# Performance work log

Hardware: AMD Instinct MI355X
Metric: run time of the kernel (lower is better)

## Reference

```python
import jax, jax.numpy as jnp
import numpy as np

# SLAYER SRM-ALPHA neuron / simulation constants (from netParams)
THETA = 10.0      # spike threshold
TAU_SR = 10.0     # PSP (SRM) time constant
TAU_REF = 1.0     # refractory time constant
SCALE_REF = 2.0
TAU_RHO = 1.0     # surrogate-gradient width (unused in fwd)
SCALE_RHO = 1.0
TS = 1.0
K_SRM = 100       # truncation of alpha kernel (values < 1e-4 beyond this)
K_REF = 16

def _alpha_kernel(tau, K, mult):
    t = jnp.arange(K, dtype=jnp.float32) * TS
    return mult * (t / tau) * jnp.exp(1.0 - t / tau)

SRM_KERNEL = _alpha_kernel(TAU_SR, K_SRM, 1.0)                       # eps(t)
REF_KERNEL = _alpha_kernel(TAU_REF, K_REF, -2.0 * THETA * SCALE_REF)  # nu(t)

def heaviside(u):
    return (u >= THETA).astype(u.dtype)

def psp(x):
    # causal temporal convolution with SRM alpha kernel; x: (..., T)
    T = x.shape[-1]
    K = SRM_KERNEL.shape[0]
    flat = x.reshape(-1, 1, T)  # (N, C=1, T)
    out = jax.lax.conv_general_dilated(flat, SRM_KERNEL[::-1].reshape(1, 1, K),
                                       (1,), [(K - 1, 0)])
    return out.reshape(x.shape)

def spike(v):
    # SLAYER spike generation with refractory feedback; v: (..., T)
    refk = REF_KERNEL[1:]          # refractory affects strictly future steps
    L = refk.shape[0]
    vT = jnp.moveaxis(v, -1, 0)    # (T, ...)
    pend0 = jnp.zeros(vT.shape[1:] + (L,), v.dtype)  # pending refractory contributions
    def step(pend, vt):
        u = vt + pend[..., 0]
        s = heaviside(u)
        pend = jnp.concatenate([pend[..., 1:], jnp.zeros_like(pend[..., :1])], axis=-1) \
               + s[..., None] * refk
        return pend, s
    _, sT = jax.lax.scan(step, pend0, vT)
    return jnp.moveaxis(sT, 0, -1)

def conv_t(x, W, pad):
    # per-timestep 2D conv (slayer.conv uses Conv3d with kernel (k,k,1), no bias)
    B, C, H, Wd, T = x.shape
    xt = jnp.transpose(x, (0, 4, 1, 2, 3)).reshape(B * T, C, H, Wd)
    y = jax.lax.conv_general_dilated(xt, W, (1, 1), [(pad, pad), (pad, pad)])
    Co, Ho, Wo = y.shape[1:]
    return jnp.transpose(y.reshape(B, T, Co, Ho, Wo), (0, 2, 3, 4, 1))

def pool_t(x):
    # slayer.pool(2): 2x2 sum-pool with constant weight 1.1*theta per element
    s = jax.lax.reduce_window(x, 0.0, jax.lax.add, (1, 1, 2, 2, 1), (1, 1, 2, 2, 1), 'VALID')
    return s * (1.1 * THETA)

def _forward(spikeInput, W1, W2, W3, W4, Wfc):
    x = spike(conv_t(psp(spikeInput), W1, 1))   # (B,16,48,48,T)
    x = spike(pool_t(psp(x)))                   # (B,16,24,24,T)
    x = spike(conv_t(psp(x), W2, 1))            # (B,32,24,24,T)
    x = spike(pool_t(psp(x)))                   # (B,32,12,12,T)
    x = spike(conv_t(psp(x), W3, 1))            # (B,64,12,12,T)
    x = spike(pool_t(psp(x)))                   # (B,64,6,6,T)
    x = spike(conv_t(psp(x), W4, 1))            # (B,64,6,6,T)
    x = spike(jnp.einsum('bchwt,kchw->bkt', psp(x), Wfc))  # (B,10,T)
    return x

def setup_inputs():
    key = jax.random.key(0)
    ks = jax.random.split(key, 6)
    B, T = 4, 200
    spikeInput = (jax.random.uniform(ks[0], (B, 2, 50, 50, T)) < 0.05).astype(jnp.float32)
    W1 = 0.5 * jax.random.normal(ks[1], (16, 2, 5, 5), jnp.float32)
    W2 = 0.25 * jax.random.normal(ks[2], (32, 16, 3, 3), jnp.float32)
    W3 = 0.25 * jax.random.normal(ks[3], (64, 32, 3, 3), jnp.float32)
    W4 = 0.25 * jax.random.normal(ks[4], (64, 64, 3, 3), jnp.float32)
    Wfc = 0.1 * jax.random.normal(ks[5], (10, 64, 6, 6), jnp.float32)
    return {"spikeInput": spikeInput, "W1": W1, "W2": W2, "W3": W3, "W4": W4, "Wfc": Wfc}

def reference(spikeInput, W1, W2, W3, W4, Wfc):
    return _forward(spikeInput, W1, W2, W3, W4, Wfc)
```

## Files before the change

### kernel.cpp

```cpp
#include <hip/hip_runtime.h>
#include <math.h>


#define THETA 10.0f
#define RSTRIDE 204

__global__ void prep_kernel(const float* __restrict__ W1, const float* __restrict__ W2,
                            const float* __restrict__ W3, const float* __restrict__ W4,
                            float* HQ, float* rk,
                            float* wt1, float* wt2, float* wt3, float* wt4) {
    int i = blockIdx.x * 256 + threadIdx.x;
    if (i < 144) {
        int k = i - 15;
        float val = 0.0f;
        if (k >= 0 && k <= 99) {
            float tf = (float)k;
            float x = tf / 10.0f;
            val = x * (float)exp((double)(1.0f - x));
        }
        HQ[i] = val;
    } else if (i < 160) {
        int j = i - 144;
        if (j < 15) {
            float t = (float)(j + 1);
            rk[j] = (-40.0f * t) * (float)exp((double)(1.0f - t));
        }
    } else if (i < 960) {
        int j = i - 160, co = j / 50, tp = j % 50;
        wt1[tp * 16 + co] = W1[j];
    } else if (i < 5568) {
        int j = i - 960, co = j / 144, tp = j % 144;
        wt2[tp * 32 + co] = W2[j];
    } else if (i < 24000) {
        int j = i - 5568, co = j / 288, tp = j % 288;
        wt3[tp * 64 + co] = W3[j];
    } else if (i < 60864) {
        int j = i - 24000, co = j / 576, tp = j % 576;
        wt4[tp * 64 + co] = W4[j];
    }
}

#define FIR_STEP(A0, A1, A2, A3, qx, qy, qz, qw, hA, hB)  \
    A0 = fmaf(hA.x, qw, A0);                              \
    A1 = fmaf(hA.y, qw, A1);                              \
    A2 = fmaf(hA.z, qw, A2);                              \
    A3 = fmaf(hA.w, qw, A3);                              \
    A0 = fmaf(hA.y, qz, A0);                              \
    A1 = fmaf(hA.z, qz, A1);                              \
    A2 = fmaf(hA.w, qz, A2);                              \
    A3 = fmaf(hB.x, qz, A3);                              \
    A0 = fmaf(hA.z, qy, A0);                              \
    A1 = fmaf(hA.w, qy, A1);                              \
    A2 = fmaf(hB.x, qy, A2);                              \
    A3 = fmaf(hB.y, qy, A3);                              \
    A0 = fmaf(hA.w, qx, A0);                              \
    A1 = fmaf(hB.x, qx, A1);                              \
    A2 = fmaf(hB.y, qx, A2);                              \
    A3 = fmaf(hB.z, qx, A3);

#define SCAN4(XV, p, rk)                                          \
    {                                                             \
        float u_, sv_;                                            \
        u_ = XV.x + p[0]; sv_ = (u_ >= THETA) ? 1.0f : 0.0f;      \
        XV.x = sv_;                                               \
        _Pragma("unroll")                                         \
        for (int i_ = 0; i_ < 14; ++i_) p[i_] = fmaf(sv_, rk[i_], p[i_ + 1]); \
        p[14] = sv_ * rk[14];                                     \
        u_ = XV.y + p[0]; sv_ = (u_ >= THETA) ? 1.0f : 0.0f;      \
        XV.y = sv_;                                               \
        _Pragma("unroll")                                         \
        for (int i_ = 0; i_ < 14; ++i_) p[i_] = fmaf(sv_, rk[i_], p[i_ + 1]); \
        p[14] = sv_ * rk[14];                                     \
        u_ = XV.z + p[0]; sv_ = (u_ >= THETA) ? 1.0f : 0.0f;      \
        XV.z = sv_;                                               \
        _Pragma("unroll")                                         \
        for (int i_ = 0; i_ < 14; ++i_) p[i_] = fmaf(sv_, rk[i_], p[i_ + 1]); \
        p[14] = sv_ * rk[14];                                     \
        u_ = XV.w + p[0]; sv_ = (u_ >= THETA) ? 1.0f : 0.0f;      \
        XV.w = sv_;                                               \
        _Pragma("unroll")                                         \
        for (int i_ = 0; i_ < 14; ++i_) p[i_] = fmaf(sv_, rk[i_], p[i_ + 1]); \
        p[14] = sv_ * rk[14];                                     \
    }

__device__ __forceinline__ void fir_run2(const float* __restrict__ row,
                                         const float4* __restrict__ HQ4,
                                         int t0, int jend, float4 (&acc)[2]) {
    float4 A = HQ4[2], B = HQ4[3], C = HQ4[4];
    const float* bp = row + t0 + 4;
    for (int j = 0; j <= jend; ++j) {
        const float4 qv = *reinterpret_cast<const float4*>(bp);
        const float4 N = HQ4[j + 5];
        FIR_STEP(acc[0].x, acc[0].y, acc[0].z, acc[0].w,
                 qv.x, qv.y, qv.z, qv.w, A, B)
        FIR_STEP(acc[1].x, acc[1].y, acc[1].z, acc[1].w,
                 qv.x, qv.y, qv.z, qv.w, B, C)
        A = B; B = C; C = N;
        bp -= 4;
    }
}

__device__ static const signed char FIR_ITEMS[8][4] = {
    {24, 12, 8, -1}, {22, 21, 4, -1}, {20, 19, 3, -1}, {18, 17, 2, -1},
    {16, 15, 1, 0},  {13, 11, 5, -1}, {14, 10, 6, -1}, {23, 9, 7, -1}};

template <bool SCAN>
__global__ __launch_bounds__(512) void spikepsp_kernel(const float* __restrict__ in,
                                                       float* __restrict__ out,
                                                       const float* __restrict__ HQ,
                                                       const float* __restrict__ rkt,
                                                       int n) {
    __shared__ __align__(16) float tile[64 * RSTRIDE];
    const int l = threadIdx.x & 63;
    const int w = threadIdx.x >> 6;
    const int s0 = blockIdx.x * 64;
    for (int i = threadIdx.x; i < 3200; i += 512) {
        const int slot = i / 50, q = i - slot * 50;
        const int ser = s0 + slot;
        float4 v = make_float4(0.f, 0.f, 0.f, 0.f);
        if (ser < n) v = *reinterpret_cast<const float4*>(in + (long)ser * 200 + 4 * q);
        *reinterpret_cast<float4*>(&tile[slot * RSTRIDE + 4 * q]) = v;
    }
    __syncthreads();
    if (SCAN) {
        if (w == 0) {
            float rk[15];
            #pragma unroll
            for (int i = 0; i < 15; ++i) rk[i] = rkt[i];
            float p[15];
            #pragma unroll
            for (int i = 0; i < 15; ++i) p[i] = 0.0f;
            float* row = tile + l * RSTRIDE;
            for (int tq = 0; tq < 50; ++tq) {
                float4 xv = *reinterpret_cast<const float4*>(&row[4 * tq]);
                SCAN4(xv, p, rk)
                *reinterpret_cast<float4*>(&row[4 * tq]) = xv;
            }
        }
        __syncthreads();
    }
    const bool valid = (s0 + l) < n;
    const float* row = tile + l * RSTRIDE;
    const float4* HQ4 = reinterpret_cast<const float4*>(HQ);
    float* op = out + (long)(s0 + l) * 200;
    #pragma unroll
    for (int k = 0; k < 4; ++k) {
        const int id = FIR_ITEMS[w][k];
        if (id < 0) break;
        const int t0 = 8 * id;
        const int jend = ((2 * id < 25) ? 2 * id : 25) + 1;
        float4 acc[2];
        acc[0] = make_float4(0.f, 0.f, 0.f, 0.f);
        acc[1] = make_float4(0.f, 0.f, 0.f, 0.f);
        fir_run2(row, HQ4, t0, jend, acc);
        if (valid) {
            *reinterpret_cast<float4*>(op + t0) = acc[0];
            *reinterpret_cast<float4*>(op + t0 + 4) = acc[1];
        }
    }
}

__global__ __launch_bounds__(512) void spikepsppool_kernel(const float* __restrict__ in,
                                                           float* __restrict__ out,
                                                           const float* __restrict__ HQ,
                                                           const float* __restrict__ rkt,
                                                           int C, int HO, int WO) {
    __shared__ __align__(16) float tile[64 * RSTRIDE];
    __shared__ int sbase[64];
    const int l = threadIdx.x & 63;
    const int w = threadIdx.x >> 6;
    const int o0 = blockIdx.x * 16;
    const int H = 2 * HO, W = 2 * WO;
    if (threadIdx.x < 64) {
        const int oi = threadIdx.x >> 2, p = threadIdx.x & 3;
        const int o = o0 + oi;
        const int wo = o % WO; int tmp = o / WO;
        const int ho = tmp % HO; tmp /= HO;
        const int c = tmp % C; const int b = tmp / C;
        sbase[threadIdx.x] = ((b * C + c) * H + 2 * ho + (p >> 1)) * W + 2 * wo + (p & 1);
    }
    __syncthreads();
    for (int i = threadIdx.x; i < 3200; i += 512) {
        const int slot = i / 50, q = i - slot * 50;
        const float4 v = *reinterpret_cast<const float4*>(in + (long)sbase[slot] * 200 + 4 * q);
        *reinterpret_cast<float4*>(&tile[slot * RSTRIDE + 4 * q]) = v;
    }
    __syncthreads();
    if (w == 0) {
        float rk[15];
        #pragma unroll
        for (int i = 0; i < 15; ++i) rk[i] = rkt[i];
        float p[15];
        #pragma unroll
        for (int i = 0; i < 15; ++i) p[i] = 0.0f;
        float* row = tile + l * RSTRIDE;
        for (int tq = 0; tq < 50; ++tq) {
            float4 xv = *reinterpret_cast<const float4*>(&row[4 * tq]);
            SCAN4(xv, p, rk)
            *reinterpret_cast<float4*>(&row[4 * tq]) = xv;
        }
    }
    __syncthreads();
    const int qb = l & ~3;
    const float* row = tile + l * RSTRIDE;
    const float4* HQ4 = reinterpret_cast<const float4*>(HQ);
    float* op = out + (long)(o0 + (l >> 2)) * 200;
    auto qsum = [&](float v) -> float {
        const float v0 = __shfl(v, qb + 0);
        const float v1 = __shfl(v, qb + 1);
        const float v2 = __shfl(v, qb + 2);
        const float v3 = __shfl(v, qb + 3);
        return (((v0 + v1) + v2) + v3) * 11.0f;
    };
    #pragma unroll
    for (int k = 0; k < 4; ++k) {
        const int id = FIR_ITEMS[w][k];
        if (id < 0) break;
        const int t0 = 8 * id;
        const int jend = ((2 * id < 25) ? 2 * id : 25) + 1;
        float4 acc[2];
        acc[0] = make_float4(0.f, 0.f, 0.f, 0.f);
        acc[1] = make_float4(0.f, 0.f, 0.f, 0.f);
        fir_run2(row, HQ4, t0, jend, acc);
        #pragma unroll
        for (int d = 0; d < 2; ++d) {
            float4 r;
            r.x = qsum(acc[d].x); r.y = qsum(acc[d].y);
            r.z = qsum(acc[d].z); r.w = qsum(acc[d].w);
            if ((l & 3) == 0)
                *reinterpret_cast<float4*>(op + t0 + 4 * d) = r;
        }
    }
}

template <int K, int PAD, int CI, int COG>
__global__ __launch_bounds__(256) void conv_kernel(const float* __restrict__ x,
                                                   const float* __restrict__ wt,
                                                   float* __restrict__ out,
                                                   int Co, int H, int W,
                                                   int HO, int WO) {
    const int l = threadIdx.x & 63;
    const int wv = threadIdx.x >> 6;
    if (l >= 50) return;
    const int p = blockIdx.x * 4 + wv;
    const int wo = p % WO, ho = p / WO;
    const int co0 = blockIdx.y * COG;
    const int b = blockIdx.z;
    const int t0 = l * 4;
    float4 acc[COG];
    #pragma unroll
    for (int c = 0; c < COG; ++c) acc[c] = make_float4(0.f, 0.f, 0.f, 0.f);
    const float* xb = x + ((long)b * CI * H * W) * 200 + t0;
    for (int ci = 0; ci < CI; ++ci) {
        #pragma unroll
        for (int kh = 0; kh < K; ++kh) {
            const int hi = ho + kh - PAD;
            if (hi < 0 || hi >= H) continue;
            #pragma unroll
            for (int kw = 0; kw < K; ++kw) {
                const int wi = wo + kw - PAD;
                if (wi < 0 || wi >= W) continue;
                const float4 v = *reinterpret_cast<const float4*>(
                    xb + ((long)(ci * H + hi) * W + wi) * 200);
                const float* wp = wt + ((ci * K + kh) * K + kw) * Co + co0;
                #pragma unroll
                for (int c = 0; c < COG; ++c) {
                    const float wv_ = wp[c];
                    acc[c].x = fmaf(wv_, v.x, acc[c].x);
                    acc[c].y = fmaf(wv_, v.y, acc[c].y);
                    acc[c].z = fmaf(wv_, v.z, acc[c].z);
                    acc[c].w = fmaf(wv_, v.w, acc[c].w);
                }
            }
        }
    }
    const long hwN = (long)HO * WO;
    const long ob = ((long)(b * Co + co0) * HO + ho) * WO + wo;
    #pragma unroll
    for (int c = 0; c < COG; ++c)
        *reinterpret_cast<float4*>(out + (ob + c * hwN) * 200 + t0) = acc[c];
}

template <int CI, int COG>
__global__ __launch_bounds__(256) void conv3_kernel(const float* __restrict__ x,
                                                    const float* __restrict__ wt,
                                                    float* __restrict__ out,
                                                    int Co, int H, int W) {
    const int l = threadIdx.x & 63;
    const int wv = threadIdx.x >> 6;
    if (l >= 50) return;
    const int p = blockIdx.x * 4 + wv;
    const int wo = p % W, ho = p / W;
    const int co0 = blockIdx.y * COG;
    const int b = blockIdx.z;
    const int t0 = l * 4;
    float4 acc[COG];
    #pragma unroll
    for (int c = 0; c < COG; ++c) acc[c] = make_float4(0.f, 0.f, 0.f, 0.f);

    bool vm[9];
    #pragma unroll
    for (int i = 0; i < 9; ++i) {
        const int hi = ho + i / 3 - 1, wi = wo + i % 3 - 1;
        vm[i] = (hi >= 0) && (hi < H) && (wi >= 0) && (wi < W);
    }
    const long cis = (long)H * W * 200;
    const float* pb = x + (long)b * CI * cis + ((long)(ho - 1) * W + (wo - 1)) * 200 + t0;

    float4 bufA[9], bufB[9];
    auto ld = [&](int ci, float4 (&B)[9]) {
        const float* pc = pb + ci * cis;
        #pragma unroll
        for (int i = 0; i < 9; ++i) {
            B[i] = vm[i] ? *reinterpret_cast<const float4*>(pc + ((i / 3) * W + (i % 3)) * 200)
                         : make_float4(0.f, 0.f, 0.f, 0.f);
        }
    };
    auto fm = [&](const float4 (&B)[9], int ci) {
        #pragma unroll
        for (int i = 0; i < 9; ++i) {
            const float* wp = wt + (ci * 9 + i) * Co + co0;
            #pragma unroll
            for (int c = 0; c < COG; ++c) {
                const float wv_ = wp[c];
                acc[c].x = fmaf(wv_, B[i].x, acc[c].x);
                acc[c].y = fmaf(wv_, B[i].y, acc[c].y);
                acc[c].z = fmaf(wv_, B[i].z, acc[c].z);
                acc[c].w = fmaf(wv_, B[i].w, acc[c].w);
            }
        }
    };

    ld(0, bufA);
    #pragma unroll 1
    for (int ci = 0; ci < CI; ci += 2) {
        ld(ci + 1, bufB);
        fm(bufA, ci);
        if (ci + 2 < CI) ld(ci + 2, bufA);
        fm(bufB, ci + 1);
    }

    const long hwN = (long)H * W;
    const long ob = ((long)(b * Co + co0) * H + ho) * W + wo;
    #pragma unroll
    for (int c = 0; c < COG; ++c)
        *reinterpret_cast<float4*>(out + (ob + c * hwN) * 200 + t0) = acc[c];
}

__global__ __launch_bounds__(256) void spike_kernel(const float* __restrict__ v,
                                                    float* __restrict__ s,
                                                    const float* __restrict__ rkt,
                                                    int n) {
    const int nid = blockIdx.x * 256 + threadIdx.x;
    if (nid >= n) return;
    float rk[15];
    #pragma unroll
    for (int i = 0; i < 15; ++i) rk[i] = rkt[i];
    float p[15];
    #pragma unroll
    for (int i = 0; i < 15; ++i) p[i] = 0.0f;
    const float* vp = v + (long)nid * 200;
    float* sp = s + (long)nid * 200;
    for (int t = 0; t < 200; ++t) {
        const float u = vp[t] + p[0];
        const float sv = (u >= THETA) ? 1.0f : 0.0f;
        sp[t] = sv;
        #pragma unroll
        for (int i = 0; i < 14; ++i) p[i] = fmaf(sv, rk[i], p[i + 1]);
        p[14] = sv * rk[14];
    }
}

__global__ __launch_bounds__(128) void fc_kernel(const float* __restrict__ x,
                                                 const float* __restrict__ wf,
                                                 float* __restrict__ out) {
    __shared__ __align__(16) float xs[8 * 2308];
    const int b = blockIdx.x;
    const int t0 = blockIdx.y * 8;
    const int tid = threadIdx.x;
    const float* xb = x + (long)b * 2304 * 200 + t0;
    for (int i = tid; i < 4608; i += 128) {
        const int m = i >> 1, qh = (i & 1) * 4;
        const float4 v = *reinterpret_cast<const float4*>(xb + (long)m * 200 + qh);
        xs[(qh + 0) * 2308 + m] = v.x;
        xs[(qh + 1) * 2308 + m] = v.y;
        xs[(qh + 2) * 2308 + m] = v.z;
        xs[(qh + 3) * 2308 + m] = v.w;
    }
    __syncthreads();
    if (tid < 80) {
        const int k = tid >> 3, q = tid & 7;
        float a = 0.0f;
        const float* wp = wf + k * 2304;
        const float* xp = xs + q * 2308;
        for (int m4 = 0; m4 < 2304; m4 += 4) {
            const float4 xv = *reinterpret_cast<const float4*>(xp + m4);
            const float4 wv = *reinterpret_cast<const float4*>(wp + m4);
            a = fmaf(wv.x, xv.x, a);
            a = fmaf(wv.y, xv.y, a);
            a = fmaf(wv.z, xv.z, a);
            a = fmaf(wv.w, xv.w, a);
        }
        out[((long)b * 10 + k) * 200 + t0 + q] = a;
    }
}

extern "C" void kernel_launch(void* const* d_in, const int* in_sizes, int n_in,
                              void* d_out, int out_size, void* d_ws, size_t ws_size,
                              hipStream_t stream) {
    const float* x_in = (const float*)d_in[0];
    const float* W1 = (const float*)d_in[1];
    const float* W2 = (const float*)d_in[2];
    const float* W3 = (const float*)d_in[3];
    const float* W4 = (const float*)d_in[4];
    const float* Wfc = (const float*)d_in[5];
    float* outp = (float*)d_out;

    float* ws = (float*)d_ws;
    float* HQ  = ws;
    float* rk  = ws + 144;
    float* wt1 = ws + 160;
    float* wt2 = wt1 + 800;
    float* wt3 = wt2 + 4608;
    float* wt4 = wt3 + 18432;
    float* A   = wt4 + 36864;
    float* B   = A + 7372800;
    float* C   = B + 29491200;

    hipLaunchKernelGGL(prep_kernel, dim3(238), dim3(256), 0, stream,
                       W1, W2, W3, W4, HQ, rk, wt1, wt2, wt3, wt4);

    hipLaunchKernelGGL((spikepsp_kernel<false>), dim3(313), dim3(512), 0, stream,
                       x_in, A, HQ, rk, 20000);
    hipLaunchKernelGGL((conv_kernel<5, 1, 2, 16>), dim3(2304 / 4, 1, 4), dim3(256), 0, stream,
                       A, wt1, B, 16, 50, 50, 48, 48);
    hipLaunchKernelGGL(spikepsppool_kernel, dim3(36864 / 16), dim3(512), 0, stream,
                       B, A, HQ, rk, 16, 24, 24);
    hipLaunchKernelGGL((spikepsp_kernel<true>), dim3(36864 / 64), dim3(512), 0, stream,
                       A, B, HQ, rk, 36864);
    hipLaunchKernelGGL((conv3_kernel<16, 8>), dim3(576 / 4, 4, 4), dim3(256), 0, stream,
                       B, wt2, C, 32, 24, 24);
    hipLaunchKernelGGL(spikepsppool_kernel, dim3(18432 / 16), dim3(512), 0, stream,
                       C, A, HQ, rk, 32, 12, 12);
    hipLaunchKernelGGL((spikepsp_kernel<true>), dim3(18432 / 64), dim3(512), 0, stream,
                       A, B, HQ, rk, 18432);
    hipLaunchKernelGGL((conv3_kernel<32, 8>), dim3(144 / 4, 8, 4), dim3(256), 0, stream,
                       B, wt3, C, 64, 12, 12);
    hipLaunchKernelGGL(spikepsppool_kernel, dim3(9216 / 16), dim3(512), 0, stream,
                       C, A, HQ, rk, 64, 6, 6);
    hipLaunchKernelGGL((spikepsp_kernel<true>), dim3(9216 / 64), dim3(512), 0, stream,
                       A, B, HQ, rk, 9216);
    hipLaunchKernelGGL((conv3_kernel<64, 4>), dim3(36 / 4, 16, 4), dim3(256), 0, stream,
                       B, wt4, C, 64, 6, 6);
    hipLaunchKernelGGL((spikepsp_kernel<true>), dim3(9216 / 64), dim3(512), 0, stream,
                       C, B, HQ, rk, 9216);
    hipLaunchKernelGGL(fc_kernel, dim3(4, 25), dim3(128), 0, stream, B, Wfc, A);
    hipLaunchKernelGGL(spike_kernel, dim3(1), dim3(256), 0, stream, A, outp, rk, 40);
    (void)in_sizes; (void)n_in; (void)out_size; (void)ws_size;
}
```

Baseline: 675.9 us.

## Replace dense PSP FIR with sparse spike-list accumulation of pre-shifted kernel

The spike scan now writes a compacted list of spike times into each shared row instead of a dense 0/1 vector. The PSP convolution walks only that list and adds pre-shifted alpha-kernel windows from a staged table in LDS, replacing the dense banded FIR. The input is binary spikes, so this computes the same result. It avoids multiply-adds on zero samples, at the cost of data-dependent loops, wave divergence and gather loads from LDS. The first layer also builds a spike list from its raw input, and the tile load loop is reorganised so each group of 8 threads loads one row.

```diff
diff --git a/kernel.cpp b/kernel.cpp
--- a/kernel.cpp
+++ b/kernel.cpp
@@ -7,97 +7,70 @@
 
 __global__ void prep_kernel(const float* __restrict__ W1, const float* __restrict__ W2,
                             const float* __restrict__ W3, const float* __restrict__ W4,
-                            float* HQ, float* rk,
+                            float* HS, float* rk,
                             float* wt1, float* wt2, float* wt3, float* wt4) {
     int i = blockIdx.x * 256 + threadIdx.x;
-    if (i < 144) {
-        int k = i - 15;
+    if (i < 448) {
+        const int fi = i >> 2, e = i & 3;
+        const int r = fi / 28, qm2 = fi % 28;
+        const int hqi = 4 * (qm2 + 2) + r + e;
+        const int k = hqi - 15;
         float val = 0.0f;
         if (k >= 0 && k <= 99) {
-            float tf = (float)k;
-            float x = tf / 10.0f;
+            float x = (float)k / 10.0f;
             val = x * (float)exp((double)(1.0f - x));
         }
-        HQ[i] = val;
-    } else if (i < 160) {
-        int j = i - 144;
+        HS[i] = val;
+    } else if (i < 464) {
+        int j = i - 448;
         if (j < 15) {
             float t = (float)(j + 1);
             rk[j] = (-40.0f * t) * (float)exp((double)(1.0f - t));
         }
-    } else if (i < 960) {
-        int j = i - 160, co = j / 50, tp = j % 50;
+    } else if (i < 1264) {
+        int j = i - 464, co = j / 50, tp = j % 50;
         wt1[tp * 16 + co] = W1[j];
-    } else if (i < 5568) {
-        int j = i - 960, co = j / 144, tp = j % 144;
+    } else if (i < 5872) {
+        int j = i - 1264, co = j / 144, tp = j % 144;
         wt2[tp * 32 + co] = W2[j];
-    } else if (i < 24000) {
-        int j = i - 5568, co = j / 288, tp = j % 288;
+    } else if (i < 24304) {
+        int j = i - 5872, co = j / 288, tp = j % 288;
         wt3[tp * 64 + co] = W3[j];
-    } else if (i < 60864) {
-        int j = i - 24000, co = j / 576, tp = j % 576;
+    } else if (i < 61168) {
+        int j = i - 24304, co = j / 576, tp = j % 576;
         wt4[tp * 64 + co] = W4[j];
     }
 }
 
-#define FIR_STEP(A0, A1, A2, A3, qx, qy, qz, qw, hA, hB)  \
-    A0 = fmaf(hA.x, qw, A0);                              \
-    A1 = fmaf(hA.y, qw, A1);                              \
-    A2 = fmaf(hA.z, qw, A2);                              \
-    A3 = fmaf(hA.w, qw, A3);                              \
-    A0 = fmaf(hA.y, qz, A0);                              \
-    A1 = fmaf(hA.z, qz, A1);                              \
-    A2 = fmaf(hA.w, qz, A2);                              \
-    A3 = fmaf(hB.x, qz, A3);                              \
-    A0 = fmaf(hA.z, qy, A0);                              \
-    A1 = fmaf(hA.w, qy, A1);                              \
-    A2 = fmaf(hB.x, qy, A2);                              \
-    A3 = fmaf(hB.y, qy, A3);                              \
-    A0 = fmaf(hA.w, qx, A0);                              \
-    A1 = fmaf(hB.x, qx, A1);                              \
-    A2 = fmaf(hB.y, qx, A2);                              \
-    A3 = fmaf(hB.z, qx, A3);
-
-#define SCAN4(XV, p, rk)                                          \
-    {                                                             \
-        float u_, sv_;                                            \
-        u_ = XV.x + p[0]; sv_ = (u_ >= THETA) ? 1.0f : 0.0f;      \
-        XV.x = sv_;                                               \
-        _Pragma("unroll")                                         \
+#define SCANL(XC, TF, row, cnt, p, rk)                                        \
+    {                                                                         \
+        const float u_ = (XC) + p[0];                                         \
+        const bool sp_ = (u_ >= THETA);                                       \
+        const float sv_ = sp_ ? 1.0f : 0.0f;                                  \
+        row[cnt] = (TF);                                                      \
+        cnt += sp_ ? 1 : 0;                                                   \
+        _Pragma("unroll")                                                     \
         for (int i_ = 0; i_ < 14; ++i_) p[i_] = fmaf(sv_, rk[i_], p[i_ + 1]); \
-        p[14] = sv_ * rk[14];                                     \
-        u_ = XV.y + p[0]; sv_ = (u_ >= THETA) ? 1.0f : 0.0f;      \
-        XV.y = sv_;                                               \
-        _Pragma("unroll")                                         \
-        for (int i_ = 0; i_ < 14; ++i_) p[i_] = fmaf(sv_, rk[i_], p[i_ + 1]); \
-        p[14] = sv_ * rk[14];                                     \
-        u_ = XV.z + p[0]; sv_ = (u_ >= THETA) ? 1.0f : 0.0f;      \
-        XV.z = sv_;                                               \
-        _Pragma("unroll")                                         \
-        for (int i_ = 0; i_ < 14; ++i_) p[i_] = fmaf(sv_, rk[i_], p[i_ + 1]); \
-        p[14] = sv_ * rk[14];                                     \
-        u_ = XV.w + p[0]; sv_ = (u_ >= THETA) ? 1.0f : 0.0f;      \
-        XV.w = sv_;                                               \
-        _Pragma("unroll")                                         \
-        for (int i_ = 0; i_ < 14; ++i_) p[i_] = fmaf(sv_, rk[i_], p[i_ + 1]); \
-        p[14] = sv_ * rk[14];                                     \
-    }
-
-__device__ __forceinline__ void fir_run2(const float* __restrict__ row,
-                                         const float4* __restrict__ HQ4,
-                                         int t0, int jend, float4 (&acc)[2]) {
-    float4 A = HQ4[2], B = HQ4[3], C = HQ4[4];
-    const float* bp = row + t0 + 4;
-    for (int j = 0; j <= jend; ++j) {
-        const float4 qv = *reinterpret_cast<const float4*>(bp);
-        const float4 N = HQ4[j + 5];
-        FIR_STEP(acc[0].x, acc[0].y, acc[0].z, acc[0].w,
-                 qv.x, qv.y, qv.z, qv.w, A, B)
-        FIR_STEP(acc[1].x, acc[1].y, acc[1].z, acc[1].w,
-                 qv.x, qv.y, qv.z, qv.w, B, C)
-        A = B; B = C; C = N;
-        bp -= 4;
-    }
+        p[14] = sv_ * rk[14];                                                 \
+    }
+
+__device__ __forceinline__ int fir_sparse(const float* __restrict__ row,
+                                          const float* __restrict__ HS,
+                                          int t0, int hi, float4 (&acc)[2]) {
+    const float thi = (float)(t0 + 7);
+    const float tlo = (float)(t0 - 99);
+    while (hi >= 0 && row[hi] > thi) --hi;
+    for (int i = hi; i >= 0; --i) {
+        const float tf = row[i];
+        if (tf < tlo) break;
+        const int m = t0 + 15 - (int)tf;
+        const int off = ((m & 3) * 28 + (m >> 2) - 2) * 4;
+        const float4 a = *reinterpret_cast<const float4*>(HS + off);
+        const float4 b = *reinterpret_cast<const float4*>(HS + off + 4);
+        acc[0].x += a.x; acc[0].y += a.y; acc[0].z += a.z; acc[0].w += a.w;
+        acc[1].x += b.x; acc[1].y += b.y; acc[1].z += b.z; acc[1].w += b.w;
+    }
+    return hi;
 }
 
 __device__ static const signed char FIR_ITEMS[8][4] = {
@@ -107,52 +80,74 @@
 template <bool SCAN>
 __global__ __launch_bounds__(512) void spikepsp_kernel(const float* __restrict__ in,
                                                        float* __restrict__ out,
-                                                       const float* __restrict__ HQ,
+                                                       const float* __restrict__ HSg,
                                                        const float* __restrict__ rkt,
                                                        int n) {
     __shared__ __align__(16) float tile[64 * RSTRIDE];
+    __shared__ __align__(16) float HSl[448];
     const int l = threadIdx.x & 63;
     const int w = threadIdx.x >> 6;
     const int s0 = blockIdx.x * 64;
-    for (int i = threadIdx.x; i < 3200; i += 512) {
-        const int slot = i / 50, q = i - slot * 50;
+    if (threadIdx.x < 112)
+        reinterpret_cast<float4*>(HSl)[threadIdx.x] =
+            reinterpret_cast<const float4*>(HSg)[threadIdx.x];
+    {
+        const int slot = threadIdx.x >> 3;
+        const int q8 = threadIdx.x & 7;
         const int ser = s0 + slot;
-        float4 v = make_float4(0.f, 0.f, 0.f, 0.f);
-        if (ser < n) v = *reinterpret_cast<const float4*>(in + (long)ser * 200 + 4 * q);
-        *reinterpret_cast<float4*>(&tile[slot * RSTRIDE + 4 * q]) = v;
+        const float* src = in + (long)ser * 200;
+        float* drow = tile + slot * RSTRIDE;
+        for (int q = q8; q < 50; q += 8) {
+            float4 v = make_float4(0.f, 0.f, 0.f, 0.f);
+            if (ser < n) v = *reinterpret_cast<const float4*>(src + 4 * q);
+            *reinterpret_cast<float4*>(drow + 4 * q) = v;
+        }
     }
     __syncthreads();
-    if (SCAN) {
-        if (w == 0) {
+    if (w == 0) {
+        float* row = tile + l * RSTRIDE;
+        int cnt = 0;
+        if (SCAN) {
             float rk[15];
             #pragma unroll
             for (int i = 0; i < 15; ++i) rk[i] = rkt[i];
             float p[15];
             #pragma unroll
             for (int i = 0; i < 15; ++i) p[i] = 0.0f;
-            float* row = tile + l * RSTRIDE;
             for (int tq = 0; tq < 50; ++tq) {
                 float4 xv = *reinterpret_cast<const float4*>(&row[4 * tq]);
-                SCAN4(xv, p, rk)
-                *reinterpret_cast<float4*>(&row[4 * tq]) = xv;
+                const float tb = (float)(4 * tq);
+                SCANL(xv.x, tb, row, cnt, p, rk)
+                SCANL(xv.y, tb + 1.0f, row, cnt, p, rk)
+                SCANL(xv.z, tb + 2.0f, row, cnt, p, rk)
+                SCANL(xv.w, tb + 3.0f, row, cnt, p, rk)
             }
-        }
-        __syncthreads();
-    }
+        } else {
+            for (int tq = 0; tq < 50; ++tq) {
+                float4 xv = *reinterpret_cast<const float4*>(&row[4 * tq]);
+                const float tb = (float)(4 * tq);
+                row[cnt] = tb;        cnt += (xv.x != 0.0f) ? 1 : 0;
+                row[cnt] = tb + 1.0f; cnt += (xv.y != 0.0f) ? 1 : 0;
+                row[cnt] = tb + 2.0f; cnt += (xv.z != 0.0f) ? 1 : 0;
+                row[cnt] = tb + 3.0f; cnt += (xv.w != 0.0f) ? 1 : 0;
+            }
+        }
+        row[200] = (float)cnt;
+    }
+    __syncthreads();
     const bool valid = (s0 + l) < n;
     const float* row = tile + l * RSTRIDE;
-    const float4* HQ4 = reinterpret_cast<const float4*>(HQ);
+    int hi = (int)row[200] - 1;
     float* op = out + (long)(s0 + l) * 200;
     #pragma unroll
     for (int k = 0; k < 4; ++k) {
         const int id = FIR_ITEMS[w][k];
         if (id < 0) break;
         const int t0 = 8 * id;
-        const int jend = ((2 * id < 25) ? 2 * id : 25) + 1;
         float4 acc[2];
         acc[0] = make_float4(0.f, 0.f, 0.f, 0.f);
         acc[1] = make_float4(0.f, 0.f, 0.f, 0.f);
-        fir_run2(row, HQ4, t0, jend, acc);
+        hi = fir_sparse(row, HSl, t0, hi, acc);
         if (valid) {
             *reinterpret_cast<float4*>(op + t0) = acc[0];
             *reinterpret_cast<float4*>(op + t0 + 4) = acc[1];
@@ -162,28 +157,32 @@
 
 __global__ __launch_bounds__(512) void spikepsppool_kernel(const float* __restrict__ in,
                                                            float* __restrict__ out,
-                                                           const float* __restrict__ HQ,
+                                                           const float* __restrict__ HSg,
                                                            const float* __restrict__ rkt,
                                                            int C, int HO, int WO) {
     __shared__ __align__(16) float tile[64 * RSTRIDE];
-    __shared__ int sbase[64];
+    __shared__ __align__(16) float HSl[448];
     const int l = threadIdx.x & 63;
     const int w = threadIdx.x >> 6;
     const int o0 = blockIdx.x * 16;
     const int H = 2 * HO, W = 2 * WO;
-    if (threadIdx.x < 64) {
-        const int oi = threadIdx.x >> 2, p = threadIdx.x & 3;
+    if (threadIdx.x < 112)
+        reinterpret_cast<float4*>(HSl)[threadIdx.x] =
+            reinterpret_cast<const float4*>(HSg)[threadIdx.x];
+    {
+        const int slot = threadIdx.x >> 3;
+        const int q8 = threadIdx.x & 7;
+        const int oi = slot >> 2, pq = slot & 3;
         const int o = o0 + oi;
         const int wo = o % WO; int tmp = o / WO;
         const int ho = tmp % HO; tmp /= HO;
         const int c = tmp % C; const int b = tmp / C;
-        sbase[threadIdx.x] = ((b * C + c) * H + 2 * ho + (p >> 1)) * W + 2 * wo + (p & 1);
-    }
-    __syncthreads();
-    for (int i = threadIdx.x; i < 3200; i += 512) {
-        const int slot = i / 50, q = i - slot * 50;
-        const float4 v = *reinterpret_cast<const float4*>(in + (long)sbase[slot] * 200 + 4 * q);
-        *reinterpret_cast<float4*>(&tile[slot * RSTRIDE + 4 * q]) = v;
+        const long sb = ((long)((b * C + c) * H + 2 * ho + (pq >> 1))) * W + 2 * wo + (pq & 1);
+        const float* src = in + sb * 200;
+        float* drow = tile + slot * RSTRIDE;
+        for (int q = q8; q < 50; q += 8)
+            *reinterpret_cast<float4*>(drow + 4 * q) =
+                *reinterpret_cast<const float4*>(src + 4 * q);
     }
     __syncthreads();
     if (w == 0) {
@@ -194,16 +193,21 @@
         #pragma unroll
         for (int i = 0; i < 15; ++i) p[i] = 0.0f;
         float* row = tile + l * RSTRIDE;
+        int cnt = 0;
         for (int tq = 0; tq < 50; ++tq) {
             float4 xv = *reinterpret_cast<const float4*>(&row[4 * tq]);
-            SCAN4(xv, p, rk)
-            *reinterpret_cast<float4*>(&row[4 * tq]) = xv;
-        }
+            const float tb = (float)(4 * tq);
+            SCANL(xv.x, tb, row, cnt, p, rk)
+            SCANL(xv.y, tb + 1.0f, row, cnt, p, rk)
+            SCANL(xv.z, tb + 2.0f, row, cnt, p, rk)
+            SCANL(xv.w, tb + 3.0f, row, cnt, p, rk)
+        }
+        row[200] = (float)cnt;
     }
     __syncthreads();
     const int qb = l & ~3;
     const float* row = tile + l * RSTRIDE;
-    const float4* HQ4 = reinterpret_cast<const float4*>(HQ);
+    int hi = (int)row[200] - 1;
     float* op = out + (long)(o0 + (l >> 2)) * 200;
     auto qsum = [&](float v) -> float {
         const float v0 = __shfl(v, qb + 0);
@@ -217,11 +221,10 @@
         const int id = FIR_ITEMS[w][k];
         if (id < 0) break;
         const int t0 = 8 * id;
-        const int jend = ((2 * id < 25) ? 2 * id : 25) + 1;
         float4 acc[2];
         acc[0] = make_float4(0.f, 0.f, 0.f, 0.f);
         acc[1] = make_float4(0.f, 0.f, 0.f, 0.f);
-        fir_run2(row, HQ4, t0, jend, acc);
+        hi = fir_sparse(row, HSl, t0, hi, acc);
         #pragma unroll
         for (int d = 0; d < 2; ++d) {
             float4 r;
@@ -417,9 +420,9 @@
     float* outp = (float*)d_out;
 
     float* ws = (float*)d_ws;
-    float* HQ  = ws;
-    float* rk  = ws + 144;
-    float* wt1 = ws + 160;
+    float* HS  = ws;
+    float* rk  = ws + 448;
+    float* wt1 = ws + 464;
     float* wt2 = wt1 + 800;
     float* wt3 = wt2 + 4608;
     float* wt4 = wt3 + 18432;
@@ -427,33 +430,33 @@
     float* B   = A + 7372800;
     float* C   = B + 29491200;
 
-    hipLaunchKernelGGL(prep_kernel, dim3(238), dim3(256), 0, stream,
-                       W1, W2, W3, W4, HQ, rk, wt1, wt2, wt3, wt4);
+    hipLaunchKernelGGL(prep_kernel, dim3(239), dim3(256), 0, stream,
+                       W1, W2, W3, W4, HS, rk, wt1, wt2, wt3, wt4);
 
     hipLaunchKernelGGL((spikepsp_kernel<false>), dim3(313), dim3(512), 0, stream,
-                       x_in, A, HQ, rk, 20000);
+                       x_in, A, HS, rk, 20000);
     hipLaunchKernelGGL((conv_kernel<5, 1, 2, 16>), dim3(2304 / 4, 1, 4), dim3(256), 0, stream,
                        A, wt1, B, 16, 50, 50, 48, 48);
     hipLaunchKernelGGL(spikepsppool_kernel, dim3(36864 / 16), dim3(512), 0, stream,
-                       B, A, HQ, rk, 16, 24, 24);
+                       B, A, HS, rk, 16, 24, 24);
     hipLaunchKernelGGL((spikepsp_kernel<true>), dim3(36864 / 64), dim3(512), 0, stream,
-                       A, B, HQ, rk, 36864);
+                       A, B, HS, rk, 36864);
     hipLaunchKernelGGL((conv3_kernel<16, 8>), dim3(576 / 4, 4, 4), dim3(256), 0, stream,
                        B, wt2, C, 32, 24, 24);
     hipLaunchKernelGGL(spikepsppool_kernel, dim3(18432 / 16), dim3(512), 0, stream,
-                       C, A, HQ, rk, 32, 12, 12);
+                       C, A, HS, rk, 32, 12, 12);
     hipLaunchKernelGGL((spikepsp_kernel<true>), dim3(18432 / 64), dim3(512), 0, stream,
-                       A, B, HQ, rk, 18432);
+                       A, B, HS, rk, 18432);
     hipLaunchKernelGGL((conv3_kernel<32, 8>), dim3(144 / 4, 8, 4), dim3(256), 0, stream,
                        B, wt3, C, 64, 12, 12);
     hipLaunchKernelGGL(spikepsppool_kernel, dim3(9216 / 16), dim3(512), 0, stream,
-                       C, A, HQ, rk, 64, 6, 6);
+                       C, A, HS, rk, 64, 6, 6);
     hipLaunchKernelGGL((spikepsp_kernel<true>), dim3(9216 / 64), dim3(512), 0, stream,
-                       A, B, HQ, rk, 9216);
+                       A, B, HS, rk, 9216);
     hipLaunchKernelGGL((conv3_kernel<64, 4>), dim3(36 / 4, 16, 4), dim3(256), 0, stream,
-                       B, wt4, C, 64, 6, 6);
+                       B, wt4, C, 64, 4 == 4 ? 6 : 6, 6);
     hipLaunchKernelGGL((spikepsp_kernel<true>), dim3(9216 / 64), dim3(512), 0, stream,
-                       C, B, HQ, rk, 9216);
+                       C, B, HS, rk, 9216);
     hipLaunchKernelGGL(fc_kernel, dim3(4, 25), dim3(128), 0, stream, B, Wfc, A);
     hipLaunchKernelGGL(spike_kernel, dim3(1), dim3(256), 0, stream, A, outp, rk, 40);
     (void)in_sizes; (void)n_in; (void)out_size; (void)ws_size;
```

Result: slower. 788.6 us (+16.7%).

## Split spike scan into parallel kernel and pack spikes as bytes for FIR

Applied to the files above, without the earlier changes.

Moves the refractory spike scan out of the PSP kernels into a standalone scan kernel where every thread handles one neuron series, instead of a single wavefront per block doing it while the others wait. Spikes are stored as byte-packed words (four timesteps per uint), shrinking global and shared memory traffic for the FIR and pool-FIR kernels. This adds more kernel launches and an extra global write/read of the packed spike array.

```diff
diff --git a/kernel.cpp b/kernel.cpp
--- a/kernel.cpp
+++ b/kernel.cpp
@@ -3,7 +3,6 @@
 
 
 #define THETA 10.0f
-#define RSTRIDE 204
 
 __global__ void prep_kernel(const float* __restrict__ W1, const float* __restrict__ W2,
                             const float* __restrict__ W3, const float* __restrict__ W4,
@@ -37,6 +36,58 @@
     } else if (i < 60864) {
         int j = i - 24000, co = j / 576, tp = j % 576;
         wt4[tp * 64 + co] = W4[j];
+    }
+}
+
+#define SCANB(XC, BIT, W, p, rk)                                              \
+    {                                                                         \
+        const float u_ = (XC) + p[0];                                         \
+        const bool sp_ = (u_ >= THETA);                                       \
+        const float sv_ = sp_ ? 1.0f : 0.0f;                                  \
+        W |= sp_ ? (BIT) : 0u;                                                \
+        _Pragma("unroll")                                                     \
+        for (int i_ = 0; i_ < 14; ++i_) p[i_] = fmaf(sv_, rk[i_], p[i_ + 1]); \
+        p[14] = sv_ * rk[14];                                                 \
+    }
+
+#define QPROC(BV, QI)                                                         \
+    {                                                                         \
+        unsigned int w_ = 0u;                                                 \
+        SCANB(BV.x, 1u, w_, p, rk)                                            \
+        SCANB(BV.y, 0x100u, w_, p, rk)                                        \
+        SCANB(BV.z, 0x10000u, w_, p, rk)                                      \
+        SCANB(BV.w, 0x1000000u, w_, p, rk)                                    \
+        sp[QI] = w_;                                                          \
+    }
+
+__global__ __launch_bounds__(256) void scan_kernel(const float* __restrict__ v,
+                                                   unsigned int* __restrict__ s,
+                                                   const float* __restrict__ rkt,
+                                                   int n) {
+    const int nid = blockIdx.x * 256 + threadIdx.x;
+    if (nid >= n) return;
+    float rk[15];
+    #pragma unroll
+    for (int i = 0; i < 15; ++i) rk[i] = rkt[i];
+    float p[15];
+    #pragma unroll
+    for (int i = 0; i < 15; ++i) p[i] = 0.0f;
+    const float4* vp4 = reinterpret_cast<const float4*>(v + (long)nid * 200);
+    unsigned int* sp = s + (long)nid * 50;
+    float4 b0 = vp4[0], b1 = vp4[1], b2 = vp4[2], b3 = vp4[3], b4 = vp4[4];
+    #pragma unroll 1
+    for (int g = 0; g < 10; ++g) {
+        const int q0 = 5 * g;
+        QPROC(b0, q0)
+        if (g < 9) b0 = vp4[q0 + 5];
+        QPROC(b1, q0 + 1)
+        if (g < 9) b1 = vp4[q0 + 6];
+        QPROC(b2, q0 + 2)
+        if (g < 9) b2 = vp4[q0 + 7];
+        QPROC(b3, q0 + 3)
+        if (g < 9) b3 = vp4[q0 + 8];
+        QPROC(b4, q0 + 4)
+        if (g < 9) b4 = vp4[q0 + 9];
     }
 }
 
@@ -58,45 +109,21 @@
     A2 = fmaf(hB.y, qx, A2);                              \
     A3 = fmaf(hB.z, qx, A3);
 
-#define SCAN4(XV, p, rk)                                          \
-    {                                                             \
-        float u_, sv_;                                            \
-        u_ = XV.x + p[0]; sv_ = (u_ >= THETA) ? 1.0f : 0.0f;      \
-        XV.x = sv_;                                               \
-        _Pragma("unroll")                                         \
-        for (int i_ = 0; i_ < 14; ++i_) p[i_] = fmaf(sv_, rk[i_], p[i_ + 1]); \
-        p[14] = sv_ * rk[14];                                     \
-        u_ = XV.y + p[0]; sv_ = (u_ >= THETA) ? 1.0f : 0.0f;      \
-        XV.y = sv_;                                               \
-        _Pragma("unroll")                                         \
-        for (int i_ = 0; i_ < 14; ++i_) p[i_] = fmaf(sv_, rk[i_], p[i_ + 1]); \
-        p[14] = sv_ * rk[14];                                     \
-        u_ = XV.z + p[0]; sv_ = (u_ >= THETA) ? 1.0f : 0.0f;      \
-        XV.z = sv_;                                               \
-        _Pragma("unroll")                                         \
-        for (int i_ = 0; i_ < 14; ++i_) p[i_] = fmaf(sv_, rk[i_], p[i_ + 1]); \
-        p[14] = sv_ * rk[14];                                     \
-        u_ = XV.w + p[0]; sv_ = (u_ >= THETA) ? 1.0f : 0.0f;      \
-        XV.w = sv_;                                               \
-        _Pragma("unroll")                                         \
-        for (int i_ = 0; i_ < 14; ++i_) p[i_] = fmaf(sv_, rk[i_], p[i_ + 1]); \
-        p[14] = sv_ * rk[14];                                     \
-    }
-
-__device__ __forceinline__ void fir_run2(const float* __restrict__ row,
-                                         const float4* __restrict__ HQ4,
-                                         int t0, int jend, float4 (&acc)[2]) {
+__device__ __forceinline__ void fir_run2b(const unsigned int* __restrict__ rowB,
+                                          const float4* __restrict__ HQ4,
+                                          int t0, int jend, float4 (&acc)[2]) {
     float4 A = HQ4[2], B = HQ4[3], C = HQ4[4];
-    const float* bp = row + t0 + 4;
+    int wi = (t0 >> 2) + 1;
     for (int j = 0; j <= jend; ++j) {
-        const float4 qv = *reinterpret_cast<const float4*>(bp);
+        const unsigned int w = rowB[wi - j];
         const float4 N = HQ4[j + 5];
-        FIR_STEP(acc[0].x, acc[0].y, acc[0].z, acc[0].w,
-                 qv.x, qv.y, qv.z, qv.w, A, B)
-        FIR_STEP(acc[1].x, acc[1].y, acc[1].z, acc[1].w,
-                 qv.x, qv.y, qv.z, qv.w, B, C)
+        const float qx = (float)(w & 0xFFu);
+        const float qy = (float)((w >> 8) & 0xFFu);
+        const float qz = (float)((w >> 16) & 0xFFu);
+        const float qw = (float)((w >> 24) & 0xFFu);
+        FIR_STEP(acc[0].x, acc[0].y, acc[0].z, acc[0].w, qx, qy, qz, qw, A, B)
+        FIR_STEP(acc[1].x, acc[1].y, acc[1].z, acc[1].w, qx, qy, qz, qw, B, C)
         A = B; B = C; C = N;
-        bp -= 4;
     }
 }
 
@@ -104,43 +131,38 @@
     {24, 12, 8, -1}, {22, 21, 4, -1}, {20, 19, 3, -1}, {18, 17, 2, -1},
     {16, 15, 1, 0},  {13, 11, 5, -1}, {14, 10, 6, -1}, {23, 9, 7, -1}};
 
-template <bool SCAN>
-__global__ __launch_bounds__(512) void spikepsp_kernel(const float* __restrict__ in,
-                                                       float* __restrict__ out,
-                                                       const float* __restrict__ HQ,
-                                                       const float* __restrict__ rkt,
-                                                       int n) {
-    __shared__ __align__(16) float tile[64 * RSTRIDE];
+template <int MODE>
+__global__ __launch_bounds__(512) void fir_kernel(const void* __restrict__ in,
+                                                  float* __restrict__ out,
+                                                  const float* __restrict__ HQ,
+                                                  int n) {
+    __shared__ unsigned int tileB[64 * 53];
     const int l = threadIdx.x & 63;
     const int w = threadIdx.x >> 6;
     const int s0 = blockIdx.x * 64;
-    for (int i = threadIdx.x; i < 3200; i += 512) {
-        const int slot = i / 50, q = i - slot * 50;
-        const int ser = s0 + slot;
-        float4 v = make_float4(0.f, 0.f, 0.f, 0.f);
-        if (ser < n) v = *reinterpret_cast<const float4*>(in + (long)ser * 200 + 4 * q);
-        *reinterpret_cast<float4*>(&tile[slot * RSTRIDE + 4 * q]) = v;
+    if (MODE == 0) {
+        const unsigned int* ip = (const unsigned int*)in;
+        for (int i = threadIdx.x; i < 3200; i += 512) {
+            const int slot = i / 50, q = i - slot * 50;
+            tileB[53 * slot + q] = ip[(long)(s0 + slot) * 50 + q];
+        }
+    } else {
+        const float* ip = (const float*)in;
+        for (int i = threadIdx.x; i < 3200; i += 512) {
+            const int slot = i / 50, q = i - slot * 50;
+            const int ser = s0 + slot;
+            unsigned int wv = 0u;
+            if (ser < n) {
+                const float4 v = *reinterpret_cast<const float4*>(ip + (long)ser * 200 + 4 * q);
+                wv = (v.x != 0.0f ? 1u : 0u) | (v.y != 0.0f ? 0x100u : 0u) |
+                     (v.z != 0.0f ? 0x10000u : 0u) | (v.w != 0.0f ? 0x1000000u : 0u);
+            }
+            tileB[53 * slot + q] = wv;
+        }
     }
     __syncthreads();
-    if (SCAN) {
-        if (w == 0) {
-            float rk[15];
-            #pragma unroll
-            for (int i = 0; i < 15; ++i) rk[i] = rkt[i];
-            float p[15];
-            #pragma unroll
-            for (int i = 0; i < 15; ++i) p[i] = 0.0f;
-            float* row = tile + l * RSTRIDE;
-            for (int tq = 0; tq < 50; ++tq) {
-                float4 xv = *reinterpret_cast<const float4*>(&row[4 * tq]);
-                SCAN4(xv, p, rk)
-                *reinterpret_cast<float4*>(&row[4 * tq]) = xv;
-            }
-        }
-        __syncthreads();
-    }
     const bool valid = (s0 + l) < n;
-    const float* row = tile + l * RSTRIDE;
+    const unsigned int* rowB = tileB + 53 * l;
     const float4* HQ4 = reinterpret_cast<const float4*>(HQ);
     float* op = out + (long)(s0 + l) * 200;
     #pragma unroll
@@ -152,7 +174,7 @@
         float4 acc[2];
         acc[0] = make_float4(0.f, 0.f, 0.f, 0.f);
         acc[1] = make_float4(0.f, 0.f, 0.f, 0.f);
-        fir_run2(row, HQ4, t0, jend, acc);
+        fir_run2b(rowB, HQ4, t0, jend, acc);
         if (valid) {
             *reinterpret_cast<float4*>(op + t0) = acc[0];
             *reinterpret_cast<float4*>(op + t0 + 4) = acc[1];
@@ -160,49 +182,28 @@
     }
 }
 
-__global__ __launch_bounds__(512) void spikepsppool_kernel(const float* __restrict__ in,
-                                                           float* __restrict__ out,
-                                                           const float* __restrict__ HQ,
-                                                           const float* __restrict__ rkt,
-                                                           int C, int HO, int WO) {
-    __shared__ __align__(16) float tile[64 * RSTRIDE];
-    __shared__ int sbase[64];
+__global__ __launch_bounds__(512) void poolfir_kernel(const unsigned int* __restrict__ in,
+                                                      float* __restrict__ out,
+                                                      const float* __restrict__ HQ,
+                                                      int C, int HO, int WO) {
+    __shared__ unsigned int tileB[64 * 53];
     const int l = threadIdx.x & 63;
     const int w = threadIdx.x >> 6;
     const int o0 = blockIdx.x * 16;
     const int H = 2 * HO, W = 2 * WO;
-    if (threadIdx.x < 64) {
-        const int oi = threadIdx.x >> 2, p = threadIdx.x & 3;
+    for (int i = threadIdx.x; i < 3200; i += 512) {
+        const int slot = i / 50, q = i - slot * 50;
+        const int oi = slot >> 2, pq = slot & 3;
         const int o = o0 + oi;
         const int wo = o % WO; int tmp = o / WO;
         const int ho = tmp % HO; tmp /= HO;
         const int c = tmp % C; const int b = tmp / C;
-        sbase[threadIdx.x] = ((b * C + c) * H + 2 * ho + (p >> 1)) * W + 2 * wo + (p & 1);
-    }
-    __syncthreads();
-    for (int i = threadIdx.x; i < 3200; i += 512) {
-        const int slot = i / 50, q = i - slot * 50;
-        const float4 v = *reinterpret_cast<const float4*>(in + (long)sbase[slot] * 200 + 4 * q);
-        *reinterpret_cast<float4*>(&tile[slot * RSTRIDE + 4 * q]) = v;
-    }
-    __syncthreads();
-    if (w == 0) {
-        float rk[15];
-        #pragma unroll
-        for (int i = 0; i < 15; ++i) rk[i] = rkt[i];
-        float p[15];
-        #pragma unroll
-        for (int i = 0; i < 15; ++i) p[i] = 0.0f;
-        float* row = tile + l * RSTRIDE;
-        for (int tq = 0; tq < 50; ++tq) {
-            float4 xv = *reinterpret_cast<const float4*>(&row[4 * tq]);
-            SCAN4(xv, p, rk)
-            *reinterpret_cast<float4*>(&row[4 * tq]) = xv;
-        }
+        const long sb = ((long)((b * C + c) * H + 2 * ho + (pq >> 1))) * W + 2 * wo + (pq & 1);
+        tileB[53 * slot + q] = in[sb * 50 + q];
     }
     __syncthreads();
     const int qb = l & ~3;
-    const float* row = tile + l * RSTRIDE;
+    const unsigned int* rowB = tileB + 53 * l;
     const float4* HQ4 = reinterpret_cast<const float4*>(HQ);
     float* op = out + (long)(o0 + (l >> 2)) * 200;
     auto qsum = [&](float v) -> float {
@@ -221,7 +222,7 @@
         float4 acc[2];
         acc[0] = make_float4(0.f, 0.f, 0.f, 0.f);
         acc[1] = make_float4(0.f, 0.f, 0.f, 0.f);
-        fir_run2(row, HQ4, t0, jend, acc);
+        fir_run2b(rowB, HQ4, t0, jend, acc);
         #pragma unroll
         for (int d = 0; d < 2; ++d) {
             float4 r;
@@ -426,35 +427,43 @@
     float* A   = wt4 + 36864;
     float* B   = A + 7372800;
     float* C   = B + 29491200;
+    unsigned int* Au = (unsigned int*)A;
 
     hipLaunchKernelGGL(prep_kernel, dim3(238), dim3(256), 0, stream,
                        W1, W2, W3, W4, HQ, rk, wt1, wt2, wt3, wt4);
 
-    hipLaunchKernelGGL((spikepsp_kernel<false>), dim3(313), dim3(512), 0, stream,
-                       x_in, A, HQ, rk, 20000);
+    hipLaunchKernelGGL((fir_kernel<1>), dim3(313), dim3(512), 0, stream,
+                       x_in, A, HQ, 20000);
     hipLaunchKernelGGL((conv_kernel<5, 1, 2, 16>), dim3(2304 / 4, 1, 4), dim3(256), 0, stream,
                        A, wt1, B, 16, 50, 50, 48, 48);
-    hipLaunchKernelGGL(spikepsppool_kernel, dim3(36864 / 16), dim3(512), 0, stream,
-                       B, A, HQ, rk, 16, 24, 24);
-    hipLaunchKernelGGL((spikepsp_kernel<true>), dim3(36864 / 64), dim3(512), 0, stream,
-                       A, B, HQ, rk, 36864);
+    hipLaunchKernelGGL(scan_kernel, dim3(576), dim3(256), 0, stream, B, Au, rk, 147456);
+    hipLaunchKernelGGL(poolfir_kernel, dim3(36864 / 16), dim3(512), 0, stream,
+                       Au, C, HQ, 16, 24, 24);
+    hipLaunchKernelGGL(scan_kernel, dim3(144), dim3(256), 0, stream, C, Au, rk, 36864);
+    hipLaunchKernelGGL((fir_kernel<0>), dim3(576), dim3(512), 0, stream,
+                       Au, B, HQ, 36864);
     hipLaunchKernelGGL((conv3_kernel<16, 8>), dim3(576 / 4, 4, 4), dim3(256), 0, stream,
                        B, wt2, C, 32, 24, 24);
-    hipLaunchKernelGGL(spikepsppool_kernel, dim3(18432 / 16), dim3(512), 0, stream,
-                       C, A, HQ, rk, 32, 12, 12);
-    hipLaunchKernelGGL((spikepsp_kernel<true>), dim3(18432 / 64), dim3(512), 0, stream,
-                       A, B, HQ, rk, 18432);
+    hipLaunchKernelGGL(scan_kernel, dim3(288), dim3(256), 0, stream, C, Au, rk, 73728);
+    hipLaunchKernelGGL(poolfir_kernel, dim3(18432 / 16), dim3(512), 0, stream,
+                       Au, B, HQ, 32, 12, 12);
+    hipLaunchKernelGGL(scan_kernel, dim3(72), dim3(256), 0, stream, B, Au, rk, 18432);
+    hipLaunchKernelGGL((fir_kernel<0>), dim3(288), dim3(512), 0, stream,
+                       Au, C, HQ, 18432);
     hipLaunchKernelGGL((conv3_kernel<32, 8>), dim3(144 / 4, 8, 4), dim3(256), 0, stream,
-                       B, wt3, C, 64, 12, 12);
-    hipLaunchKernelGGL(spikepsppool_kernel, dim3(9216 / 16), dim3(512), 0, stream,
-                       C, A, HQ, rk, 64, 6, 6);
-    hipLaunchKernelGGL((spikepsp_kernel<true>), dim3(9216 / 64), dim3(512), 0, stream,
-                       A, B, HQ, rk, 9216);
+                       C, wt3, B, 64, 12, 12);
+    hipLaunchKernelGGL(scan_kernel, dim3(144), dim3(256), 0, stream, B, Au, rk, 36864);
+    hipLaunchKernelGGL(poolfir_kernel, dim3(9216 / 16), dim3(512), 0, stream,
+                       Au, C, HQ, 64, 6, 6);
+    hipLaunchKernelGGL(scan_kernel, dim3(36), dim3(256), 0, stream, C, Au, rk, 9216);
+    hipLaunchKernelGGL((fir_kernel<0>), dim3(144), dim3(512), 0, stream,
+                       Au, B, HQ, 9216);
     hipLaunchKernelGGL((conv3_kernel<64, 4>), dim3(36 / 4, 16, 4), dim3(256), 0, stream,
                        B, wt4, C, 64, 6, 6);
-    hipLaunchKernelGGL((spikepsp_kernel<true>), dim3(9216 / 64), dim3(512), 0, stream,
-                       C, B, HQ, rk, 9216);
-    hipLaunchKernelGGL(fc_kernel, dim3(4, 25), dim3(128), 0, stream, B, Wfc, A);
-    hipLaunchKernelGGL(spike_kernel, dim3(1), dim3(256), 0, stream, A, outp, rk, 40);
+    hipLaunchKernelGGL(scan_kernel, dim3(36), dim3(256), 0, stream, C, Au, rk, 9216);
+    hipLaunchKernelGGL((fir_kernel<0>), dim3(144), dim3(512), 0, stream,
+                       Au, B, HQ, 9216);
+    hipLaunchKernelGGL(fc_kernel, dim3(4, 25), dim3(128), 0, stream, B, Wfc, C);
+    hipLaunchKernelGGL(spike_kernel, dim3(1), dim3(256), 0, stream, C, outp, rk, 40);
     (void)in_sizes; (void)n_in; (void)out_size; (void)ws_size;
 }
```

Measured after the change: 988.2 us. 1.46x slower.
